# Performance work log

Measured on AMD Instinct MI355X. Metric: run time of the kernel, lower is better.

## Reference

```python
import jax, jax.numpy as jnp
import numpy as np

B, S, D = 2, 2048, 1024
E, K = 8, 2
CAP_FACTOR = 1.25
HID = 4 * D


def _capacity(num_tokens: int) -> int:
    import math
    cap = math.floor(K * CAP_FACTOR * num_tokens / E)
    cap += cap % 2
    return max(int(cap), 2)


def setup_inputs() -> dict:
    key = jax.random.key(0)
    k1, k2, k3, k4 = jax.random.split(key, 4)
    x = jax.random.normal(k1, (B, S, D), dtype=jnp.float32)
    w_gate = jax.random.normal(k2, (D, E), dtype=jnp.float32) * 0.02
    w_fc = jax.random.normal(k3, (E, D, HID), dtype=jnp.float32) * 0.02
    w_proj = jax.random.normal(k4, (E, HID, D), dtype=jnp.float32) * 0.02
    return {"x": x, "w_gate": w_gate, "w_fc": w_fc, "w_proj": w_proj}


def _moe_forward(x, w_gate, w_fc, w_proj):
    b, s, d = x.shape
    T = b * s
    cap = _capacity(T)
    xf = x.astype(jnp.float32).reshape(T, d)

    # --- Router (fp32, eval mode: no noise) ---
    logits = xf @ w_gate                                   # [T, E]
    top_v, top_i = jax.lax.top_k(logits, K)                # [T, K]
    NEG = jnp.float32(-1e30)
    masked = jnp.full_like(logits, NEG)
    masked = masked.at[jnp.arange(T)[:, None], top_i].set(top_v)
    probs = jax.nn.softmax(masked, axis=-1)                # [T, E], zero off top-k

    # --- Capacity assignment: cumsum over (k-major, token) flattened order ---
    oh = jax.nn.one_hot(top_i, E, dtype=jnp.int32)         # [T, K, E]
    oh = jnp.transpose(oh, (1, 0, 2))                      # [K, T, E]
    rank = jnp.cumsum(oh.reshape(K * T, E), axis=0).reshape(K, T, E) - 1
    within = (oh > 0) & (rank < cap)                       # [K, T, E]
    rank_sel = jnp.sum(jnp.where(within, rank, 0), axis=-1)  # [K, T]
    kept = jnp.any(within, axis=-1)                        # [K, T]

    p = jnp.take_along_axis(probs, top_i, axis=-1).T       # [K, T]
    w = jnp.where(kept, p, 0.0)                            # combine weights

    e_idx = top_i.T                                        # [K, T]
    t_idx = jnp.broadcast_to(jnp.arange(T)[None, :], (K, T))

    # expert_weights[t, e, c] (sparse scatter == torch one-hot combine)
    expert_weights = jnp.zeros((T, E, cap), jnp.float32)
    expert_weights = expert_weights.at[t_idx.ravel(), e_idx.ravel(), rank_sel.ravel()].add(w.ravel())

    # dispatch: expert_batches[e, c, :] = x of token routed to (e, c)
    disp = jnp.where(kept, 1.0, 0.0).ravel()[:, None]      # [K*T, 1]
    expert_batches = jnp.zeros((E, cap, d), jnp.float32)
    expert_batches = expert_batches.at[e_idx.ravel(), rank_sel.ravel()].add(disp * xf[t_idx.ravel()])

    # --- Expert MLPs (batched GEMMs, exact GELU, no bias, eval dropout) ---
    h = jnp.einsum('ecd,edh->ech', expert_batches, w_fc)
    h = jax.nn.gelu(h, approximate=False)
    expert_out = jnp.einsum('ech,ehd->ecd', h, w_proj)      # [E, cap, d]

    # --- Combine: gather expert outputs back to tokens weighted by router prob ---
    gathered = expert_out[e_idx.ravel(), rank_sel.ravel()].reshape(K, T, d)
    out_flat = jnp.sum(w[:, :, None] * gathered, axis=0)    # [T, d]
    output = out_flat.reshape(b, s, d)

    # --- Load balance loss (Switch) ---
    probs_full = jax.nn.softmax(logits, axis=-1)
    prob_per_expert = jnp.mean(probs_full, axis=0)          # [E]
    tokens_per_expert = jax.lax.stop_gradient(
        jnp.sum((expert_weights > 0).astype(jnp.float32), axis=(0, 2)) / (T * K)
    )
    lb_loss = E * jnp.sum(prob_per_expert * tokens_per_expert)

    # --- Router z-loss ---
    z_loss = jnp.mean(jax.nn.logsumexp(logits, axis=-1) ** 2)
    return output, lb_loss, z_loss


def reference(x, w_gate, w_fc, w_proj):
    return _moe_forward(x, w_gate, w_fc, w_proj)
```

## Files before the change

### kernel.cpp

```cpp
#include <hip/hip_runtime.h>
#include <hip/hip_bf16.h>
#include <cstdint>
#include <cstddef>

#define T_TOK 4096
#define D_DIM 1024
#define E_EXP 8
#define KSEL 2
#define CAP 1280
#define HID_DIM 4096

typedef __attribute__((ext_vector_type(8))) __bf16 bf16x8;
typedef __attribute__((ext_vector_type(8))) unsigned short ushort8;
typedef __attribute__((ext_vector_type(4))) float floatx4;

__device__ __forceinline__ unsigned short f2bf(float f) {
  unsigned int u = __builtin_bit_cast(unsigned int, f);
  u = (u + 0x7FFFu + ((u >> 16) & 1u)) >> 16;
  return (unsigned short)u;
}
__device__ __forceinline__ float bf2f(unsigned short h) {
  unsigned int u = ((unsigned int)h) << 16;
  return __builtin_bit_cast(float, u);
}

__device__ __forceinline__ void async16(const unsigned short* g, unsigned short* l) {
  __builtin_amdgcn_global_load_lds(
      (const __attribute__((address_space(1))) unsigned int*)g,
      (__attribute__((address_space(3))) unsigned int*)l, 16, 0, 0);
}

__global__ void router_kernel(const float* __restrict__ x, const float* __restrict__ wg,
                              int* __restrict__ top1, int* __restrict__ top2,
                              float* __restrict__ p0, float* __restrict__ p1,
                              float* __restrict__ probsum, float* __restrict__ zsum) {
  __shared__ float lps[E_EXP];
  __shared__ float lz;
  if (threadIdx.x < E_EXP) lps[threadIdx.x] = 0.f;
  if (threadIdx.x == 0) lz = 0.f;
  __syncthreads();
  int wave = threadIdx.x >> 6;
  int lane = threadIdx.x & 63;
  int t = blockIdx.x * 4 + wave;
  const float* xr = x + (size_t)t * D_DIM;
  float acc[E_EXP];
#pragma unroll
  for (int e = 0; e < E_EXP; ++e) acc[e] = 0.f;
  for (int j = 0; j < D_DIM / 64; ++j) {
    int i = lane + 64 * j;
    float xv = xr[i];
    const float4* wr = (const float4*)(wg + (size_t)i * E_EXP);
    float4 w0 = wr[0], w1 = wr[1];
    acc[0] += xv * w0.x; acc[1] += xv * w0.y; acc[2] += xv * w0.z; acc[3] += xv * w0.w;
    acc[4] += xv * w1.x; acc[5] += xv * w1.y; acc[6] += xv * w1.z; acc[7] += xv * w1.w;
  }
#pragma unroll
  for (int e = 0; e < E_EXP; ++e) {
#pragma unroll
    for (int s = 32; s > 0; s >>= 1) acc[e] += __shfl_xor(acc[e], s);
  }
  if (lane == 0) {
    int i1 = 0; float v1 = acc[0];
    for (int e = 1; e < E_EXP; ++e) if (acc[e] > v1) { v1 = acc[e]; i1 = e; }
    int i2 = -1; float v2 = -1e30f;
    for (int e = 0; e < E_EXP; ++e) if (e != i1 && acc[e] > v2) { v2 = acc[e]; i2 = e; }
    top1[t] = i1; top2[t] = i2;
    float dexp = expf(v2 - v1);
    p0[t] = 1.f / (1.f + dexp);
    p1[t] = dexp / (1.f + dexp);
    float pe[E_EXP]; float ssum = 0.f;
    for (int e = 0; e < E_EXP; ++e) { pe[e] = expf(acc[e] - v1); ssum += pe[e]; }
    float lse = logf(ssum) + v1;
    atomicAdd(&lz, lse * lse);
    float inv = 1.f / ssum;
    for (int e = 0; e < E_EXP; ++e) atomicAdd(&lps[e], pe[e] * inv);
  }
  __syncthreads();
  if (threadIdx.x < E_EXP) atomicAdd(&probsum[threadIdx.x], lps[threadIdx.x]);
  if (threadIdx.x == 0) atomicAdd(zsum, lz);
}

__global__ void scan_kernel(const int* __restrict__ top1, const int* __restrict__ top2,
                            int* __restrict__ rank0, int* __restrict__ rank1,
                            int* __restrict__ slot_token, int* __restrict__ cntk) {
  __shared__ int sc[256][E_EXP];
  int c = threadIdx.x;
  int e0l[16], e1l[16];
  int c0[E_EXP], c1[E_EXP];
#pragma unroll
  for (int e = 0; e < E_EXP; ++e) { c0[e] = 0; c1[e] = 0; }
#pragma unroll
  for (int j = 0; j < 16; ++j) {
    int t = c * 16 + j;
    int a = top1[t]; int b = top2[t];
    e0l[j] = a; e1l[j] = b;
    c0[a]++; c1[b]++;
  }
  for (int e = 0; e < E_EXP; ++e) sc[c][e] = c0[e];
  __syncthreads();
  for (int s = 1; s < 256; s <<= 1) {
    int tmp[E_EXP];
    if (c >= s) { for (int e = 0; e < E_EXP; ++e) tmp[e] = sc[c - s][e]; }
    __syncthreads();
    if (c >= s) { for (int e = 0; e < E_EXP; ++e) sc[c][e] += tmp[e]; }
    __syncthreads();
  }
  int off0[E_EXP], tot0[E_EXP];
  for (int e = 0; e < E_EXP; ++e) {
    off0[e] = (c > 0) ? sc[c - 1][e] : 0;
    tot0[e] = sc[255][e];
  }
  __syncthreads();
  for (int e = 0; e < E_EXP; ++e) sc[c][e] = c1[e];
  __syncthreads();
  for (int s = 1; s < 256; s <<= 1) {
    int tmp[E_EXP];
    if (c >= s) { for (int e = 0; e < E_EXP; ++e) tmp[e] = sc[c - s][e]; }
    __syncthreads();
    if (c >= s) { for (int e = 0; e < E_EXP; ++e) sc[c][e] += tmp[e]; }
    __syncthreads();
  }
  int off1[E_EXP], tot1[E_EXP];
  for (int e = 0; e < E_EXP; ++e) {
    off1[e] = (c > 0) ? sc[c - 1][e] : 0;
    tot1[e] = sc[255][e];
  }
  int run[E_EXP];
  for (int e = 0; e < E_EXP; ++e) run[e] = off0[e];
#pragma unroll
  for (int j = 0; j < 16; ++j) {
    int t = c * 16 + j;
    int e = e0l[j];
    int r = run[e]++;
    if (r < CAP) { rank0[t] = r; slot_token[e * CAP + r] = t; } else rank0[t] = -1;
  }
  for (int e = 0; e < E_EXP; ++e) run[e] = tot0[e] + off1[e];
#pragma unroll
  for (int j = 0; j < 16; ++j) {
    int t = c * 16 + j;
    int e = e1l[j];
    int r = run[e]++;
    if (r < CAP) { rank1[t] = r; slot_token[e * CAP + r] = t; } else rank1[t] = -1;
  }
  if (c == 0) {
    for (int e = 0; e < E_EXP; ++e) {
      int tot = tot0[e] + tot1[e];
      cntk[e] = tot < CAP ? tot : CAP;
    }
  }
}

__global__ void dispatch_kernel(const float* __restrict__ x, const int* __restrict__ slot_token,
                                unsigned short* __restrict__ batch) {
  int slot = blockIdx.x;
  int t = slot_token[slot];
  int d = threadIdx.x * 4;
  ushort4 o;
  if (t >= 0) {
    float4 v = *(const float4*)(x + (size_t)t * D_DIM + d);
    o.x = f2bf(v.x); o.y = f2bf(v.y); o.z = f2bf(v.z); o.w = f2bf(v.w);
  } else {
    o.x = 0; o.y = 0; o.z = 0; o.w = 0;
  }
  *(ushort4*)(batch + (size_t)slot * D_DIM + d) = o;
}

__global__ __launch_bounds__(256) void transpose_convert(const float* __restrict__ in,
                                                         unsigned short* __restrict__ out,
                                                         int R, int C) {
  __shared__ float tile[64][65];
  int b = blockIdx.z;
  int c0 = blockIdx.x * 64;
  int r0 = blockIdx.y * 64;
  const float* ip = in + (size_t)b * R * C;
  unsigned short* op = out + (size_t)b * R * C;
  int tid = threadIdx.x;
  int rr = tid >> 4;
  int cc = (tid & 15) * 4;
#pragma unroll
  for (int it = 0; it < 4; ++it) {
    int r = rr + it * 16;
    float4 v = *(const float4*)(ip + (size_t)(r0 + r) * C + c0 + cc);
    tile[r][cc] = v.x; tile[r][cc + 1] = v.y; tile[r][cc + 2] = v.z; tile[r][cc + 3] = v.w;
  }
  __syncthreads();
  int c = tid >> 2;
  int rq = (tid & 3) * 16;
  unsigned short vals[16];
#pragma unroll
  for (int j = 0; j < 16; ++j) vals[j] = f2bf(tile[rq + j][c]);
  unsigned short* dst = op + (size_t)(c0 + c) * R + r0 + rq;
  *(ushort8*)dst = *(ushort8*)&vals[0];
  *(ushort8*)(dst + 8) = *(ushort8*)&vals[8];
}

template <int KD, int NN, int NG_TILES, bool GELU>
__global__ __launch_bounds__(256) void gemm_alds(const unsigned short* __restrict__ A,
                                                 const unsigned short* __restrict__ BT,
                                                 unsigned short* __restrict__ Cd,
                                                 const int* __restrict__ cntk) {
  constexpr int MT = CAP / 128;
  constexpr int GRP = MT * NG_TILES;
  int bid = blockIdx.x;
  int e = bid & 7;
  int slot = bid >> 3;
  int ng = slot / GRP;
  int rem = slot - ng * GRP;
  int mm = rem / NG_TILES;
  int nw = rem - mm * NG_TILES;
  int m0 = mm * 128;
  int n0 = (ng * NG_TILES + nw) * 128;
  if (m0 >= cntk[e]) return;
  const unsigned short* Ae = A + (size_t)e * CAP * KD;
  const unsigned short* Be = BT + (size_t)e * NN * KD;
  unsigned short* Ce = Cd + (size_t)e * CAP * NN;
  __shared__ unsigned short As[128 * 32];
  __shared__ unsigned short Bs[128 * 32];
  int tid = threadIdx.x;
  int lane = tid & 63;
  int wv = tid >> 6;
  int wm = (wv & 1) * 64;
  int wn = (wv >> 1) * 64;
  int mrow = lane & 15;
  int kqb = lane >> 4;
  int sx = (mrow >> 1) & 3;
  int kb = (kqb ^ sx) * 8;
  floatx4 acc[4][4];
#pragma unroll
  for (int i = 0; i < 4; ++i)
#pragma unroll
    for (int j = 0; j < 4; ++j) {
      floatx4 z = {0.f, 0.f, 0.f, 0.f};
      acc[i][j] = z;
    }
  for (int k0 = 0; k0 < KD; k0 += 32) {
#pragma unroll
    for (int i = 0; i < 2; ++i) {
      int chw = i * 256 + wv * 64;
      int ch = chw + lane;
      int r = ch >> 2;
      int cbs = (ch & 3) ^ ((r >> 1) & 3);
      async16(&Ae[(size_t)(m0 + r) * KD + k0 + cbs * 8], &As[chw * 8]);
      async16(&Be[(size_t)(n0 + r) * KD + k0 + cbs * 8], &Bs[chw * 8]);
    }
    __syncthreads();
    bf16x8 af[4], bfr[4];
#pragma unroll
    for (int mt = 0; mt < 4; ++mt)
      af[mt] = *(const bf16x8*)(&As[(wm + mt * 16 + mrow) * 32 + kb]);
#pragma unroll
    for (int nt = 0; nt < 4; ++nt)
      bfr[nt] = *(const bf16x8*)(&Bs[(wn + nt * 16 + mrow) * 32 + kb]);
#pragma unroll
    for (int mt = 0; mt < 4; ++mt)
#pragma unroll
      for (int nt = 0; nt < 4; ++nt)
        acc[mt][nt] = __builtin_amdgcn_mfma_f32_16x16x32_bf16(af[mt], bfr[nt], acc[mt][nt], 0, 0, 0);
    __syncthreads();
  }
  int crow = (lane >> 4) * 4;
  int ccol = lane & 15;
#pragma unroll
  for (int mt = 0; mt < 4; ++mt)
#pragma unroll
    for (int nt = 0; nt < 4; ++nt)
#pragma unroll
      for (int r = 0; r < 4; ++r) {
        float v = acc[mt][nt][r];
        if (GELU) v = 0.5f * v * (1.f + erff(v * 0.70710678118654752f));
        Ce[(size_t)(m0 + wm + mt * 16 + crow + r) * NN + (n0 + wn + nt * 16 + ccol)] = f2bf(v);
      }
}

__global__ void combine_kernel(const unsigned short* __restrict__ EO,
                               const int* __restrict__ top1, const int* __restrict__ top2,
                               const float* __restrict__ p0, const float* __restrict__ p1,
                               const int* __restrict__ rank0, const int* __restrict__ rank1,
                               float* __restrict__ out) {
  int t = blockIdx.x;
  int d = threadIdx.x * 4;
  float a0 = 0.f, a1 = 0.f, a2 = 0.f, a3 = 0.f;
  int r0 = rank0[t];
  if (r0 >= 0) {
    float w = p0[t];
    ushort4 v = *(const ushort4*)(EO + ((size_t)top1[t] * CAP + r0) * D_DIM + d);
    a0 += w * bf2f(v.x); a1 += w * bf2f(v.y); a2 += w * bf2f(v.z); a3 += w * bf2f(v.w);
  }
  int r1 = rank1[t];
  if (r1 >= 0) {
    float w = p1[t];
    ushort4 v = *(const ushort4*)(EO + ((size_t)top2[t] * CAP + r1) * D_DIM + d);
    a0 += w * bf2f(v.x); a1 += w * bf2f(v.y); a2 += w * bf2f(v.z); a3 += w * bf2f(v.w);
  }
  float4 o; o.x = a0; o.y = a1; o.z = a2; o.w = a3;
  *(float4*)(out + (size_t)t * D_DIM + d) = o;
}

__global__ void finalize_kernel(const float* __restrict__ probsum, const float* __restrict__ zsum,
                                const int* __restrict__ cntk, float* __restrict__ out) {
  if (threadIdx.x == 0) {
    float lb = 0.f;
    for (int e = 0; e < E_EXP; ++e)
      lb += (probsum[e] / (float)T_TOK) * ((float)cntk[e] / (float)(T_TOK * KSEL));
    out[(size_t)T_TOK * D_DIM] = lb * (float)E_EXP;
    out[(size_t)T_TOK * D_DIM + 1] = zsum[0] / (float)T_TOK;
  }
}

extern "C" void kernel_launch(void* const* d_in, const int* in_sizes, int n_in,
                              void* d_out, int out_size, void* d_ws, size_t ws_size,
                              hipStream_t stream) {
  const float* x = (const float*)d_in[0];
  const float* w_gate = (const float*)d_in[1];
  const float* w_fc = (const float*)d_in[2];
  const float* w_proj = (const float*)d_in[3];
  float* out = (float*)d_out;
  char* ws = (char*)d_ws;

  float* probsum = (float*)(ws + 0);
  float* zsum    = (float*)(ws + 32);
  int*   cntk    = (int*)(ws + 64);
  int*   top1    = (int*)(ws + 4096);
  int*   top2    = (int*)(ws + 20480);
  float* p0      = (float*)(ws + 36864);
  float* p1      = (float*)(ws + 53248);
  int*   rank0   = (int*)(ws + 69632);
  int*   rank1   = (int*)(ws + 86016);
  int*   slot    = (int*)(ws + 102400);
  unsigned short* batch = (unsigned short*)(ws + 262144);
  unsigned short* H     = (unsigned short*)(ws + 262144 + 20971520);
  unsigned short* EO    = (unsigned short*)(ws + 262144 + 20971520 + 83886080);
  unsigned short* W     = (unsigned short*)(ws + 262144 + 20971520 + 83886080 + 20971520);

  hipMemsetAsync(ws, 0, 4096, stream);
  hipMemsetAsync(slot, 0xFF, E_EXP * CAP * sizeof(int), stream);

  router_kernel<<<T_TOK / 4, 256, 0, stream>>>(x, w_gate, top1, top2, p0, p1, probsum, zsum);
  scan_kernel<<<1, 256, 0, stream>>>(top1, top2, rank0, rank1, slot, cntk);
  dispatch_kernel<<<E_EXP * CAP, 256, 0, stream>>>(x, slot, batch);

  transpose_convert<<<dim3(HID_DIM / 64, D_DIM / 64, E_EXP), 256, 0, stream>>>(w_fc, W, D_DIM, HID_DIM);
  gemm_alds<D_DIM, HID_DIM, 4, true><<<8 * (HID_DIM / 128 / 4) * (CAP / 128) * 4, 256, 0, stream>>>(batch, W, H, cntk);

  transpose_convert<<<dim3(D_DIM / 64, HID_DIM / 64, E_EXP), 256, 0, stream>>>(w_proj, W, HID_DIM, D_DIM);
  gemm_alds<HID_DIM, D_DIM, 2, false><<<8 * (D_DIM / 128 / 2) * (CAP / 128) * 2, 256, 0, stream>>>(H, W, EO, cntk);

  combine_kernel<<<T_TOK, 256, 0, stream>>>(EO, top1, top2, p0, p1, rank0, rank1, out);
  finalize_kernel<<<1, 64, 0, stream>>>(probsum, zsum, cntk, out);
}
```

Baseline: 584.3 us.

## Replace expert GEMM with 256x256 tiled, 8-wave, double-buffered ping-pong pipeline

The expert GEMM kernel moves from 128x128 tiles on 4 waves to 256x256 tiles on 8 waves (512 threads). It double-buffers LDS over K in half-steps of 32 and issues async global-to-LDS loads two steps ahead. MFMA bursts run at raised priority and are bracketed by barriers and scheduling fences. The aim is to overlap memory traffic with MFMA work and to reuse each staged tile across more output. The cost is higher register and LDS use per block. Larger tiles also leave fewer blocks and coarser skipping of empty capacity rows.

```diff
diff --git a/kernel.cpp b/kernel.cpp
--- a/kernel.cpp
+++ b/kernel.cpp
@@ -194,74 +194,150 @@
   *(ushort8*)(dst + 8) = *(ushort8*)&vals[8];
 }
 
-template <int KD, int NN, int NG_TILES, bool GELU>
-__global__ __launch_bounds__(256) void gemm_alds(const unsigned short* __restrict__ A,
+template <int KD, int NN, bool GELU>
+__global__ __launch_bounds__(512, 2) void gemm8p(const unsigned short* __restrict__ A,
                                                  const unsigned short* __restrict__ BT,
                                                  unsigned short* __restrict__ Cd,
                                                  const int* __restrict__ cntk) {
-  constexpr int MT = CAP / 128;
-  constexpr int GRP = MT * NG_TILES;
+  constexpr int NT = KD / 64;
+  constexpr int MT = CAP / 256;
+  __shared__ unsigned short As[2][2][256][32];
+  __shared__ unsigned short Bs[2][2][256][32];
   int bid = blockIdx.x;
   int e = bid & 7;
   int slot = bid >> 3;
-  int ng = slot / GRP;
-  int rem = slot - ng * GRP;
-  int mm = rem / NG_TILES;
-  int nw = rem - mm * NG_TILES;
-  int m0 = mm * 128;
-  int n0 = (ng * NG_TILES + nw) * 128;
+  int mm = slot % MT;
+  int nn = slot / MT;
+  int m0 = mm * 256, n0 = nn * 256;
   if (m0 >= cntk[e]) return;
-  const unsigned short* Ae = A + (size_t)e * CAP * KD;
-  const unsigned short* Be = BT + (size_t)e * NN * KD;
+  const unsigned short* Ae = A + (size_t)e * CAP * KD + (size_t)m0 * KD;
+  const unsigned short* Be = BT + (size_t)e * NN * KD + (size_t)n0 * KD;
   unsigned short* Ce = Cd + (size_t)e * CAP * NN;
-  __shared__ unsigned short As[128 * 32];
-  __shared__ unsigned short Bs[128 * 32];
-  int tid = threadIdx.x;
-  int lane = tid & 63;
-  int wv = tid >> 6;
-  int wm = (wv & 1) * 64;
-  int wn = (wv >> 1) * 64;
-  int mrow = lane & 15;
-  int kqb = lane >> 4;
-  int sx = (mrow >> 1) & 3;
-  int kb = (kqb ^ sx) * 8;
-  floatx4 acc[4][4];
-#pragma unroll
-  for (int i = 0; i < 4; ++i)
-#pragma unroll
-    for (int j = 0; j < 4; ++j) {
-      floatx4 z = {0.f, 0.f, 0.f, 0.f};
-      acc[i][j] = z;
+  const int tid = threadIdx.x;
+  const int lane = tid & 63;
+  const int wv = tid >> 6;
+  const int wm = (wv >> 2) * 128;
+  const int wn = (wv & 3) * 64;
+  const int mrow = lane & 15;
+  const int fb = ((lane >> 4) ^ ((mrow >> 1) & 3)) * 8;
+  const int r0c = tid >> 2;
+  const int lb0 = (tid & 3) ^ ((r0c >> 1) & 3);
+  const int ld0 = (wv * 64) * 8;
+  const int ld1 = (512 + wv * 64) * 8;
+
+  floatx4 acc[8][4];
+#pragma unroll
+  for (int i = 0; i < 8; ++i)
+#pragma unroll
+    for (int j = 0; j < 4; ++j) { floatx4 z = {0.f, 0.f, 0.f, 0.f}; acc[i][j] = z; }
+
+#define STAGE_H(dst, g)                                         \
+  do {                                                          \
+    const unsigned short* _s = (g) + (size_t)r0c * KD + lb0 * 8;\
+    async16(_s, (dst) + ld0);                                   \
+    async16(_s + (size_t)128 * KD, (dst) + ld1);                \
+  } while (0)
+
+  STAGE_H(&Bs[0][0][0][0], Be);
+  asm volatile("" ::: "memory");
+  STAGE_H(&As[0][0][0][0], Ae);
+  asm volatile("" ::: "memory");
+  STAGE_H(&Bs[0][1][0][0], Be + 32);
+  asm volatile("" ::: "memory");
+  STAGE_H(&As[0][1][0][0], Ae + 32);
+  asm volatile("" ::: "memory");
+  STAGE_H(&Bs[1][0][0][0], Be + 64);
+  asm volatile("" ::: "memory");
+  STAGE_H(&As[1][0][0][0], Ae + 64);
+  asm volatile("" ::: "memory");
+  STAGE_H(&Bs[1][1][0][0], Be + 96);
+  asm volatile("s_waitcnt vmcnt(6)" ::: "memory");
+  __builtin_amdgcn_s_barrier();
+
+  bf16x8 af[4], bf[4];
+  for (int u = 0; u < NT; ++u) {
+    const int b = u & 1;
+    asm volatile("" ::: "memory");
+#pragma unroll
+    for (int m = 0; m < 4; ++m)
+      af[m] = *(const bf16x8*)&As[b][0][wm + m * 16 + mrow][fb];
+#pragma unroll
+    for (int n = 0; n < 4; ++n)
+      bf[n] = *(const bf16x8*)&Bs[b][0][wn + n * 16 + mrow][fb];
+    if (u + 1 < NT) STAGE_H(&As[b ^ 1][1][0][0], Ae + (size_t)(u + 1) * 64 + 32);
+    __builtin_amdgcn_s_barrier();
+    asm volatile("s_waitcnt lgkmcnt(0)" ::: "memory");
+    __builtin_amdgcn_sched_barrier(0);
+    __builtin_amdgcn_s_setprio(1);
+#pragma unroll
+    for (int m = 0; m < 4; ++m)
+#pragma unroll
+      for (int n = 0; n < 4; ++n)
+        acc[m][n] = __builtin_amdgcn_mfma_f32_16x16x32_bf16(af[m], bf[n], acc[m][n], 0, 0, 0);
+    __builtin_amdgcn_s_setprio(0);
+    __builtin_amdgcn_s_barrier();
+    asm volatile("" ::: "memory");
+#pragma unroll
+    for (int m = 0; m < 4; ++m)
+      af[m] = *(const bf16x8*)&As[b][0][wm + 64 + m * 16 + mrow][fb];
+    if (u + 2 < NT) STAGE_H(&Bs[b][0][0][0], Be + (size_t)(u + 2) * 64);
+    __builtin_amdgcn_s_barrier();
+    asm volatile("s_waitcnt lgkmcnt(0)" ::: "memory");
+    __builtin_amdgcn_sched_barrier(0);
+    __builtin_amdgcn_s_setprio(1);
+#pragma unroll
+    for (int m = 0; m < 4; ++m)
+#pragma unroll
+      for (int n = 0; n < 4; ++n)
+        acc[4 + m][n] = __builtin_amdgcn_mfma_f32_16x16x32_bf16(af[m], bf[n], acc[4 + m][n], 0, 0, 0);
+    __builtin_amdgcn_s_setprio(0);
+    __builtin_amdgcn_s_barrier();
+    asm volatile("" ::: "memory");
+#pragma unroll
+    for (int m = 0; m < 4; ++m)
+      af[m] = *(const bf16x8*)&As[b][1][wm + m * 16 + mrow][fb];
+#pragma unroll
+    for (int n = 0; n < 4; ++n)
+      bf[n] = *(const bf16x8*)&Bs[b][1][wn + n * 16 + mrow][fb];
+    if (u + 2 < NT) STAGE_H(&As[b][0][0][0], Ae + (size_t)(u + 2) * 64);
+    __builtin_amdgcn_s_barrier();
+    asm volatile("s_waitcnt lgkmcnt(0)" ::: "memory");
+    __builtin_amdgcn_sched_barrier(0);
+    __builtin_amdgcn_s_setprio(1);
+#pragma unroll
+    for (int m = 0; m < 4; ++m)
+#pragma unroll
+      for (int n = 0; n < 4; ++n)
+        acc[m][n] = __builtin_amdgcn_mfma_f32_16x16x32_bf16(af[m], bf[n], acc[m][n], 0, 0, 0);
+    __builtin_amdgcn_s_setprio(0);
+    __builtin_amdgcn_s_barrier();
+    asm volatile("" ::: "memory");
+#pragma unroll
+    for (int m = 0; m < 4; ++m)
+      af[m] = *(const bf16x8*)&As[b][1][wm + 64 + m * 16 + mrow][fb];
+    if (u + 2 < NT) STAGE_H(&Bs[b][1][0][0], Be + (size_t)(u + 2) * 64 + 32);
+    if (u < NT - 2) {
+      asm volatile("s_waitcnt vmcnt(6)" ::: "memory");
+    } else {
+      asm volatile("s_waitcnt vmcnt(0)" ::: "memory");
     }
-  for (int k0 = 0; k0 < KD; k0 += 32) {
-#pragma unroll
-    for (int i = 0; i < 2; ++i) {
-      int chw = i * 256 + wv * 64;
-      int ch = chw + lane;
-      int r = ch >> 2;
-      int cbs = (ch & 3) ^ ((r >> 1) & 3);
-      async16(&Ae[(size_t)(m0 + r) * KD + k0 + cbs * 8], &As[chw * 8]);
-      async16(&Be[(size_t)(n0 + r) * KD + k0 + cbs * 8], &Bs[chw * 8]);
-    }
-    __syncthreads();
-    bf16x8 af[4], bfr[4];
-#pragma unroll
-    for (int mt = 0; mt < 4; ++mt)
-      af[mt] = *(const bf16x8*)(&As[(wm + mt * 16 + mrow) * 32 + kb]);
-#pragma unroll
-    for (int nt = 0; nt < 4; ++nt)
-      bfr[nt] = *(const bf16x8*)(&Bs[(wn + nt * 16 + mrow) * 32 + kb]);
-#pragma unroll
-    for (int mt = 0; mt < 4; ++mt)
-#pragma unroll
-      for (int nt = 0; nt < 4; ++nt)
-        acc[mt][nt] = __builtin_amdgcn_mfma_f32_16x16x32_bf16(af[mt], bfr[nt], acc[mt][nt], 0, 0, 0);
-    __syncthreads();
-  }
+    __builtin_amdgcn_s_barrier();
+    asm volatile("s_waitcnt lgkmcnt(0)" ::: "memory");
+    __builtin_amdgcn_sched_barrier(0);
+    __builtin_amdgcn_s_setprio(1);
+#pragma unroll
+    for (int m = 0; m < 4; ++m)
+#pragma unroll
+      for (int n = 0; n < 4; ++n)
+        acc[4 + m][n] = __builtin_amdgcn_mfma_f32_16x16x32_bf16(af[m], bf[n], acc[4 + m][n], 0, 0, 0);
+    __builtin_amdgcn_s_setprio(0);
+    __builtin_amdgcn_s_barrier();
+  }
+#undef STAGE_H
   int crow = (lane >> 4) * 4;
   int ccol = lane & 15;
 #pragma unroll
-  for (int mt = 0; mt < 4; ++mt)
+  for (int mt = 0; mt < 8; ++mt)
 #pragma unroll
     for (int nt = 0; nt < 4; ++nt)
 #pragma unroll
@@ -340,10 +416,10 @@
   dispatch_kernel<<<E_EXP * CAP, 256, 0, stream>>>(x, slot, batch);
 
   transpose_convert<<<dim3(HID_DIM / 64, D_DIM / 64, E_EXP), 256, 0, stream>>>(w_fc, W, D_DIM, HID_DIM);
-  gemm_alds<D_DIM, HID_DIM, 4, true><<<8 * (HID_DIM / 128 / 4) * (CAP / 128) * 4, 256, 0, stream>>>(batch, W, H, cntk);
+  gemm8p<D_DIM, HID_DIM, true><<<8 * (CAP / 256) * (HID_DIM / 256), 512, 0, stream>>>(batch, W, H, cntk);
 
   transpose_convert<<<dim3(D_DIM / 64, HID_DIM / 64, E_EXP), 256, 0, stream>>>(w_proj, W, HID_DIM, D_DIM);
-  gemm_alds<HID_DIM, D_DIM, 2, false><<<8 * (D_DIM / 128 / 2) * (CAP / 128) * 2, 256, 0, stream>>>(H, W, EO, cntk);
+  gemm8p<HID_DIM, D_DIM, false><<<8 * (CAP / 256) * (D_DIM / 256), 512, 0, stream>>>(H, W, EO, cntk);
 
   combine_kernel<<<T_TOK, 256, 0, stream>>>(EO, top1, top2, p0, p1, rank0, rank1, out);
   finalize_kernel<<<1, 64, 0, stream>>>(probsum, zsum, cntk, out);
```

Measured after the change: 668.7 us. 1.14x slower.
